# Kernel optimization log

Measured on AMD Instinct MI355X. Metric: run time of the kernel, lower is better.

The kernel has to match this reference:

```python
import jax, jax.numpy as jnp
import numpy as np

NUM_NODE = 50000
NUM_REL = 50
NUM_EDGE = 1_000_000
NUM_TRI = 2_000_000
HIDDEN = 64


def setup_inputs() -> dict:
    key = jax.random.key(0)
    ks = jax.random.split(key, 9)
    rel_emb = jax.random.normal(ks[0], (NUM_REL, HIDDEN), dtype=jnp.float32)
    W_msg = jax.random.normal(ks[1], (2 * HIDDEN, HIDDEN), dtype=jnp.float32) / np.sqrt(2 * HIDDEN)
    W_upd = jax.random.normal(ks[2], (2 * HIDDEN, HIDDEN), dtype=jnp.float32) / np.sqrt(2 * HIDDEN)
    src = jax.random.randint(ks[3], (NUM_EDGE,), 0, NUM_NODE, dtype=jnp.int64 if jax.config.jax_enable_x64 else jnp.int32)
    dst = jax.random.randint(ks[4], (NUM_EDGE,), 0, NUM_NODE, dtype=src.dtype)
    rel = jax.random.randint(ks[5], (NUM_EDGE,), 0, NUM_REL, dtype=src.dtype)
    edge_ab = jax.random.randint(ks[6], (NUM_TRI,), 0, NUM_EDGE, dtype=src.dtype)
    edge_bc = jax.random.randint(ks[7], (NUM_TRI,), 0, NUM_EDGE, dtype=src.dtype)
    edge_ac = jax.random.randint(ks[8], (NUM_TRI,), 0, NUM_EDGE, dtype=src.dtype)
    return {
        "rel_emb": rel_emb, "W_msg": W_msg, "W_upd": W_upd,
        "src": src, "dst": dst, "rel": rel,
        "edge_ab": edge_ab, "edge_bc": edge_bc, "edge_ac": edge_ac,
    }


def reference(rel_emb, W_msg, W_upd, src, dst, rel, edge_ab, edge_bc, edge_ac):
    # Per-edge hidden state from relation embedding: [E, D]
    h = rel_emb[rel]
    num_edge = h.shape[0]
    # Triangle message: combine the two body edges of each grounding. [T, 2D]
    pair = jnp.concatenate([h[edge_ab], h[edge_bc]], axis=-1)
    msg = jax.nn.relu(pair @ W_msg)  # [T, D]
    # Scatter-add messages onto the head edge (a,c): irregular, memory-bound.
    agg = jax.ops.segment_sum(msg, edge_ac, num_segments=num_edge)  # [E, D]
    # Edge update.
    out = jax.nn.relu(jnp.concatenate([h, agg], axis=-1) @ W_upd)  # [E, D]
    return out
```

## Files before the change

kernel.cpp:

```cpp
#include <hip/hip_runtime.h>

#define HIDDEN 64
#define NREL 50
#define NPAIR (NREL * NREL)
#define K_SLOTS 30

typedef int   iv4 __attribute__((ext_vector_type(4)));
typedef float fv4 __attribute__((ext_vector_type(4)));

__global__ void precompute_tables(const float* __restrict__ rel_emb,
                                  const float* __restrict__ W_msg,
                                  const float* __restrict__ W_upd,
                                  const int* __restrict__ rel,
                                  unsigned char* __restrict__ rel8,
                                  int conv_n,
                                  float* __restrict__ M2,
                                  float* __restrict__ Hc) {
    const int p = blockIdx.x;
    const int j = threadIdx.x;

    for (int i = p * HIDDEN + j; i < conv_n; i += NPAIR * HIDDEN)
        rel8[i] = (unsigned char)rel[i];

    const int ra = p / NREL, rb = p % NREL;
    __shared__ float msg[HIDDEN];
    const float* ha = rel_emb + ra * HIDDEN;
    const float* hb = rel_emb + rb * HIDDEN;

    float acc = 0.f;
    #pragma unroll 8
    for (int i = 0; i < HIDDEN; ++i) acc += ha[i] * W_msg[i * HIDDEN + j];
    #pragma unroll 8
    for (int i = 0; i < HIDDEN; ++i) acc += hb[i] * W_msg[(HIDDEN + i) * HIDDEN + j];
    msg[j] = fmaxf(acc, 0.f);
    __syncthreads();

    float acc2 = 0.f;
    #pragma unroll 8
    for (int k = 0; k < HIDDEN; ++k) acc2 += msg[k] * W_upd[(HIDDEN + k) * HIDDEN + j];
    M2[p * HIDDEN + j] = acc2;

    if (p < NREL) {
        float acc3 = 0.f;
        #pragma unroll 8
        for (int i = 0; i < HIDDEN; ++i) acc3 += rel_emb[p * HIDDEN + i] * W_upd[i * HIDDEN + j];
        Hc[p * HIDDEN + j] = acc3;
    }
}

__global__ void hist_record(const unsigned char* __restrict__ rel8,
                            const int* __restrict__ edge_ab,
                            const int* __restrict__ edge_bc,
                            const int* __restrict__ edge_ac,
                            char* __restrict__ records, int num_tri) {
    const int n4 = num_tri >> 2;
    int i = blockIdx.x * blockDim.x + threadIdx.x;
    const int stride = gridDim.x * blockDim.x;
    for (; i < n4; i += stride) {
        const iv4 a = __builtin_nontemporal_load((const iv4*)edge_ab + i);
        const iv4 b = __builtin_nontemporal_load((const iv4*)edge_bc + i);
        const iv4 c = __builtin_nontemporal_load((const iv4*)edge_ac + i);
        int p[4]; char* rb[4]; int r[4];
        #pragma unroll
        for (int k = 0; k < 4; ++k) {
            p[k]  = (int)rel8[a[k]] * NREL + (int)rel8[b[k]];
            rb[k] = records + ((size_t)c[k] << 6);
        }
        #pragma unroll
        for (int k = 0; k < 4; ++k) r[k] = atomicAdd((int*)rb[k], 1);
        #pragma unroll
        for (int k = 0; k < 4; ++k)
            if (r[k] < K_SLOTS)
                *((unsigned short*)(rb[k] + 4) + r[k]) = (unsigned short)p[k];
    }
    const int rem = num_tri & 3;
    if (rem && blockIdx.x == 0 && threadIdx.x < rem) {
        const int t = (num_tri & ~3) + threadIdx.x;
        const int p = (int)rel8[edge_ab[t]] * NREL + (int)rel8[edge_bc[t]];
        char* rb = records + ((size_t)edge_ac[t] << 6);
        const int r = atomicAdd((int*)rb, 1);
        if (r < K_SLOTS) *((unsigned short*)(rb + 4) + r) = (unsigned short)p;
    }
}

__global__ void accumulate_record(const unsigned char* __restrict__ rel8,
                                  const char* __restrict__ records,
                                  const float* __restrict__ M2,
                                  const float* __restrict__ Hc,
                                  float* __restrict__ out, int num_edge) {
    const int sub = threadIdx.x >> 4;
    const int l   = threadIdx.x & 15;
    int e = blockIdx.x * 16 + sub;
    const int estride = gridDim.x * 16;
    for (; e < num_edge; e += estride) {
        const char* rec = records + ((size_t)e << 6);
        const int dc  = *(const int*)rec;
        const int deg = dc < K_SLOTS ? dc : K_SLOTS;
        const unsigned short* row = (const unsigned short*)(rec + 4);
        const int r = rel8[e];
        const fv4 h = ((const fv4*)(Hc + r * HIDDEN))[l];

        fv4 a0 = (fv4)0.f;
        fv4 a1 = (fv4)0.f;
        int k = 0;
        for (; k + 2 <= deg; k += 2) {
            const int p0 = row[k];
            const int p1 = row[k + 1];
            const fv4 m0 = ((const fv4*)M2)[p0 * 16 + l];
            const fv4 m1 = ((const fv4*)M2)[p1 * 16 + l];
            a0 += m0; a1 += m1;
        }
        if (k < deg) {
            const int p0 = row[k];
            a0 += ((const fv4*)M2)[p0 * 16 + l];
        }
        fv4 o = a0 + a1 + h;
        o.x = fmaxf(o.x, 0.f);
        o.y = fmaxf(o.y, 0.f);
        o.z = fmaxf(o.z, 0.f);
        o.w = fmaxf(o.w, 0.f);
        __builtin_nontemporal_store(o, (fv4*)out + (size_t)e * 16 + l);
    }
}

__global__ void scatter_tri(const int* __restrict__ rel,
                            const int* __restrict__ edge_ab,
                            const int* __restrict__ edge_bc,
                            const int* __restrict__ edge_ac,
                            const float* __restrict__ M2,
                            float* __restrict__ out, int num_tri) {
    const int lane   = threadIdx.x & 63;
    const int wave   = (int)((blockIdx.x * blockDim.x + threadIdx.x) >> 6);
    const int nwaves = (int)((gridDim.x * blockDim.x) >> 6);
    for (int t = wave; t < num_tri; t += nwaves) {
        const int p = rel[edge_ab[t]] * NREL + rel[edge_bc[t]];
        const float v = M2[p * HIDDEN + lane];
        unsafeAtomicAdd(&out[(size_t)edge_ac[t] * HIDDEN + lane], v);
    }
}

__global__ void finalize(const int* __restrict__ rel,
                         const float* __restrict__ Hc,
                         float* __restrict__ out, int num_edge) {
    const int total = num_edge * (HIDDEN / 4);
    int i = blockIdx.x * blockDim.x + threadIdx.x;
    const int stride = gridDim.x * blockDim.x;
    for (; i < total; i += stride) {
        const int e = i >> 4;
        const int q = i & 15;
        float4 a = ((const float4*)out)[i];
        float4 h = ((const float4*)(Hc + rel[e] * HIDDEN))[q];
        float4 o;
        o.x = fmaxf(a.x + h.x, 0.f);
        o.y = fmaxf(a.y + h.y, 0.f);
        o.z = fmaxf(a.z + h.z, 0.f);
        o.w = fmaxf(a.w + h.w, 0.f);
        ((float4*)out)[i] = o;
    }
}

extern "C" void kernel_launch(void* const* d_in, const int* in_sizes, int n_in,
                              void* d_out, int out_size, void* d_ws, size_t ws_size,
                              hipStream_t stream) {
    const float* rel_emb = (const float*)d_in[0];
    const float* W_msg   = (const float*)d_in[1];
    const float* W_upd   = (const float*)d_in[2];
    const int* rel     = (const int*)d_in[5];
    const int* edge_ab = (const int*)d_in[6];
    const int* edge_bc = (const int*)d_in[7];
    const int* edge_ac = (const int*)d_in[8];
    float* out = (float*)d_out;

    const int num_edge = in_sizes[5];
    const int num_tri  = in_sizes[6];

    char* ws = (char*)d_ws;
    size_t off = 0;
    auto alloc = [&](size_t bytes) { char* p = ws + off; off = (off + bytes + 255) & ~(size_t)255; return p; };
    float*         M2      = (float*)alloc((size_t)NPAIR * HIDDEN * 4);
    float*         Hc      = (float*)alloc((size_t)NREL * HIDDEN * 4);
    unsigned char* rel8    = (unsigned char*)alloc((size_t)num_edge);
    char*          records = (char*)alloc((size_t)num_edge * 64);
    const size_t required = off;

    const bool fast = (ws_size >= required);

    if (fast) {
        hipMemsetAsync(records, 0, (size_t)num_edge * 64, stream);
        precompute_tables<<<NPAIR, HIDDEN, 0, stream>>>(rel_emb, W_msg, W_upd,
                                                        rel, rel8, num_edge, M2, Hc);
        const int n4 = num_tri >> 2;
        int hblocks = (n4 + 255) / 256;
        if (hblocks > 4096) hblocks = 4096;
        if (hblocks < 1) hblocks = 1;
        hist_record<<<hblocks, 256, 0, stream>>>(rel8, edge_ab, edge_bc, edge_ac,
                                                 records, num_tri);
        int ablocks = (num_edge + 15) / 16;
        if (ablocks > 8192) ablocks = 8192;
        accumulate_record<<<ablocks, 256, 0, stream>>>(rel8, records, M2, Hc,
                                                       out, num_edge);
    } else {
        precompute_tables<<<NPAIR, HIDDEN, 0, stream>>>(rel_emb, W_msg, W_upd,
                                                        rel, (unsigned char*)d_ws, 0, M2, Hc);
        hipMemsetAsync(d_out, 0, (size_t)out_size * sizeof(float), stream);
        scatter_tri<<<8192, 256, 0, stream>>>(rel, edge_ab, edge_bc, edge_ac, M2, out, num_tri);
        const int total4 = num_edge * (HIDDEN / 4);
        int fin_blocks = (total4 + 255) / 256;
        if (fin_blocks > 65535 * 8) fin_blocks = 65535 * 8;
        finalize<<<fin_blocks, 256, 0, stream>>>(rel, Hc, out, num_edge);
    }
}
```

Baseline: 461.3 us.

## Split per-edge records into 16-byte inline header plus overflow array

Each edge's 64-byte record is split into a 16-byte header holding the count and six inline pair ids, plus a separate 48-byte overflow array for slots 7 to 30. Only the header is memset. The accumulate kernel reads the header with one vector load and prefetches the next edge's header. The histogram kernel now handles 8 triangles per thread and drops the block cap. The goal is less memset and record traffic, since the average degree is about 2 and most edges fit inline, at the cost of more complex indexing and a second access for high-degree edges.

Measured after the change: 473.4 us. 2.6% more time.

```diff
diff --git a/kernel.cpp b/kernel.cpp
--- a/kernel.cpp
+++ b/kernel.cpp
@@ -3,6 +3,7 @@
 #define HIDDEN 64
 #define NREL 50
 #define NPAIR (NREL * NREL)
+#define K_INL 6
 #define K_SLOTS 30
 
 typedef int   iv4 __attribute__((ext_vector_type(4)));
@@ -48,78 +49,105 @@
     }
 }
 
-__global__ void hist_record(const unsigned char* __restrict__ rel8,
-                            const int* __restrict__ edge_ab,
-                            const int* __restrict__ edge_bc,
-                            const int* __restrict__ edge_ac,
-                            char* __restrict__ records, int num_tri) {
-    const int n4 = num_tri >> 2;
+__global__ __launch_bounds__(256) void hist_record(
+        const unsigned char* __restrict__ rel8,
+        const int* __restrict__ edge_ab,
+        const int* __restrict__ edge_bc,
+        const int* __restrict__ edge_ac,
+        unsigned int* __restrict__ recA,
+        unsigned short* __restrict__ recB,
+        int num_tri) {
+    const int n8 = num_tri >> 3;
     int i = blockIdx.x * blockDim.x + threadIdx.x;
     const int stride = gridDim.x * blockDim.x;
-    for (; i < n4; i += stride) {
-        const iv4 a = __builtin_nontemporal_load((const iv4*)edge_ab + i);
-        const iv4 b = __builtin_nontemporal_load((const iv4*)edge_bc + i);
-        const iv4 c = __builtin_nontemporal_load((const iv4*)edge_ac + i);
-        int p[4]; char* rb[4]; int r[4];
+    for (; i < n8; i += stride) {
+        const iv4 a0 = __builtin_nontemporal_load((const iv4*)edge_ab + 2 * i);
+        const iv4 a1 = __builtin_nontemporal_load((const iv4*)edge_ab + 2 * i + 1);
+        const iv4 b0 = __builtin_nontemporal_load((const iv4*)edge_bc + 2 * i);
+        const iv4 b1 = __builtin_nontemporal_load((const iv4*)edge_bc + 2 * i + 1);
+        const iv4 c0 = __builtin_nontemporal_load((const iv4*)edge_ac + 2 * i);
+        const iv4 c1 = __builtin_nontemporal_load((const iv4*)edge_ac + 2 * i + 1);
+        int p[8], c[8];
         #pragma unroll
         for (int k = 0; k < 4; ++k) {
-            p[k]  = (int)rel8[a[k]] * NREL + (int)rel8[b[k]];
-            rb[k] = records + ((size_t)c[k] << 6);
-        }
+            p[k]     = (int)rel8[a0[k]] * NREL + (int)rel8[b0[k]];
+            p[k + 4] = (int)rel8[a1[k]] * NREL + (int)rel8[b1[k]];
+            c[k]     = c0[k];
+            c[k + 4] = c1[k];
+        }
+        unsigned int r[8];
         #pragma unroll
-        for (int k = 0; k < 4; ++k) r[k] = atomicAdd((int*)rb[k], 1);
+        for (int k = 0; k < 8; ++k)
+            r[k] = atomicAdd(recA + ((size_t)c[k] << 2), 1u);
         #pragma unroll
-        for (int k = 0; k < 4; ++k)
-            if (r[k] < K_SLOTS)
-                *((unsigned short*)(rb[k] + 4) + r[k]) = (unsigned short)p[k];
-    }
-    const int rem = num_tri & 3;
-    if (rem && blockIdx.x == 0 && threadIdx.x < rem) {
-        const int t = (num_tri & ~3) + threadIdx.x;
+        for (int k = 0; k < 8; ++k) {
+            if (r[k] < K_INL)
+                ((unsigned short*)(recA + ((size_t)c[k] << 2) + 1))[r[k]] = (unsigned short)p[k];
+            else if (r[k] < K_SLOTS)
+                recB[(size_t)c[k] * 24 + (r[k] - K_INL)] = (unsigned short)p[k];
+        }
+    }
+    const int rem = num_tri & 7;
+    if (rem && blockIdx.x == gridDim.x - 1 && threadIdx.x < rem) {
+        const int t = (num_tri & ~7) + threadIdx.x;
         const int p = (int)rel8[edge_ab[t]] * NREL + (int)rel8[edge_bc[t]];
-        char* rb = records + ((size_t)edge_ac[t] << 6);
-        const int r = atomicAdd((int*)rb, 1);
-        if (r < K_SLOTS) *((unsigned short*)(rb + 4) + r) = (unsigned short)p;
-    }
-}
-
-__global__ void accumulate_record(const unsigned char* __restrict__ rel8,
-                                  const char* __restrict__ records,
-                                  const float* __restrict__ M2,
-                                  const float* __restrict__ Hc,
-                                  float* __restrict__ out, int num_edge) {
+        const size_t c = (size_t)edge_ac[t];
+        const unsigned int r = atomicAdd(recA + (c << 2), 1u);
+        if (r < K_INL) ((unsigned short*)(recA + (c << 2) + 1))[r] = (unsigned short)p;
+        else if (r < K_SLOTS) recB[c * 24 + (r - K_INL)] = (unsigned short)p;
+    }
+}
+
+__global__ __launch_bounds__(256) void accumulate_record(
+        const unsigned char* __restrict__ rel8,
+        const unsigned int* __restrict__ recA,
+        const unsigned short* __restrict__ recB,
+        const float* __restrict__ M2,
+        const float* __restrict__ Hc,
+        float* __restrict__ out, int num_edge) {
     const int sub = threadIdx.x >> 4;
     const int l   = threadIdx.x & 15;
+    const int estride = gridDim.x * 16;
     int e = blockIdx.x * 16 + sub;
-    const int estride = gridDim.x * 16;
-    for (; e < num_edge; e += estride) {
-        const char* rec = records + ((size_t)e << 6);
-        const int dc  = *(const int*)rec;
+    if (e >= num_edge) return;
+    iv4 w = __builtin_nontemporal_load((const iv4*)recA + e);
+    int re = rel8[e];
+    while (true) {
+        const int en = e + estride;
+        const bool more = en < num_edge;
+        iv4 wn = {};
+        int rn = 0;
+        if (more) {
+            wn = __builtin_nontemporal_load((const iv4*)recA + en);
+            rn = rel8[en];
+        }
+        const int dc  = w.x;
         const int deg = dc < K_SLOTS ? dc : K_SLOTS;
-        const unsigned short* row = (const unsigned short*)(rec + 4);
-        const int r = rel8[e];
-        const fv4 h = ((const fv4*)(Hc + r * HIDDEN))[l];
-
-        fv4 a0 = (fv4)0.f;
-        fv4 a1 = (fv4)0.f;
-        int k = 0;
-        for (; k + 2 <= deg; k += 2) {
-            const int p0 = row[k];
-            const int p1 = row[k + 1];
-            const fv4 m0 = ((const fv4*)M2)[p0 * 16 + l];
-            const fv4 m1 = ((const fv4*)M2)[p1 * 16 + l];
-            a0 += m0; a1 += m1;
-        }
-        if (k < deg) {
-            const int p0 = row[k];
-            a0 += ((const fv4*)M2)[p0 * 16 + l];
-        }
-        fv4 o = a0 + a1 + h;
+        fv4 acc0 = ((const fv4*)(Hc + re * HIDDEN))[l];
+        fv4 acc1 = (fv4)0.f;
+        const int s0 = w.y & 0xFFFF, s1 = ((unsigned)w.y) >> 16;
+        const int s2 = w.z & 0xFFFF, s3 = ((unsigned)w.z) >> 16;
+        const int s4 = w.w & 0xFFFF, s5 = ((unsigned)w.w) >> 16;
+        if (deg > 0) acc0 += ((const fv4*)M2)[s0 * 16 + l];
+        if (deg > 1) acc1 += ((const fv4*)M2)[s1 * 16 + l];
+        if (deg > 2) acc0 += ((const fv4*)M2)[s2 * 16 + l];
+        if (deg > 3) acc1 += ((const fv4*)M2)[s3 * 16 + l];
+        if (deg > 4) acc0 += ((const fv4*)M2)[s4 * 16 + l];
+        if (deg > 5) acc1 += ((const fv4*)M2)[s5 * 16 + l];
+        if (deg > K_INL) {
+            for (int k = K_INL; k < deg; ++k) {
+                const int p = recB[(size_t)e * 24 + (k - K_INL)];
+                acc0 += ((const fv4*)M2)[p * 16 + l];
+            }
+        }
+        fv4 o = acc0 + acc1;
         o.x = fmaxf(o.x, 0.f);
         o.y = fmaxf(o.y, 0.f);
         o.z = fmaxf(o.z, 0.f);
         o.w = fmaxf(o.w, 0.f);
         __builtin_nontemporal_store(o, (fv4*)out + (size_t)e * 16 + l);
+        if (!more) break;
+        e = en; w = wn; re = rn;
     }
 }
 
@@ -177,27 +205,27 @@
     char* ws = (char*)d_ws;
     size_t off = 0;
     auto alloc = [&](size_t bytes) { char* p = ws + off; off = (off + bytes + 255) & ~(size_t)255; return p; };
-    float*         M2      = (float*)alloc((size_t)NPAIR * HIDDEN * 4);
-    float*         Hc      = (float*)alloc((size_t)NREL * HIDDEN * 4);
-    unsigned char* rel8    = (unsigned char*)alloc((size_t)num_edge);
-    char*          records = (char*)alloc((size_t)num_edge * 64);
+    float*          M2   = (float*)alloc((size_t)NPAIR * HIDDEN * 4);
+    float*          Hc   = (float*)alloc((size_t)NREL * HIDDEN * 4);
+    unsigned char*  rel8 = (unsigned char*)alloc((size_t)num_edge);
+    unsigned int*   recA = (unsigned int*)alloc((size_t)num_edge * 16);
+    unsigned short* recB = (unsigned short*)alloc((size_t)num_edge * 48);
     const size_t required = off;
 
     const bool fast = (ws_size >= required);
 
     if (fast) {
-        hipMemsetAsync(records, 0, (size_t)num_edge * 64, stream);
+        hipMemsetAsync(recA, 0, (size_t)num_edge * 16, stream);
         precompute_tables<<<NPAIR, HIDDEN, 0, stream>>>(rel_emb, W_msg, W_upd,
                                                         rel, rel8, num_edge, M2, Hc);
-        const int n4 = num_tri >> 2;
-        int hblocks = (n4 + 255) / 256;
-        if (hblocks > 4096) hblocks = 4096;
+        const int n8 = num_tri >> 3;
+        int hblocks = (n8 + 255) / 256;
         if (hblocks < 1) hblocks = 1;
         hist_record<<<hblocks, 256, 0, stream>>>(rel8, edge_ab, edge_bc, edge_ac,
-                                                 records, num_tri);
+                                                 recA, recB, num_tri);
         int ablocks = (num_edge + 15) / 16;
-        if (ablocks > 8192) ablocks = 8192;
-        accumulate_record<<<ablocks, 256, 0, stream>>>(rel8, records, M2, Hc,
+        if (ablocks > 16384) ablocks = 16384;
+        accumulate_record<<<ablocks, 256, 0, stream>>>(rel8, recA, recB, M2, Hc,
                                                        out, num_edge);
     } else {
         precompute_tables<<<NPAIR, HIDDEN, 0, stream>>>(rel_emb, W_msg, W_upd,
```
